# Kernel optimization log

Measured on AMD Instinct MI355X. Metric: run time of the kernel, lower is better.

## Reference

```python
import jax, jax.numpy as jnp
import numpy as np

NEG_INF = -1e30  # stand-in for float('-inf') masked_fill (safe for softmax)


def setup_inputs() -> dict:
    key = jax.random.key(0)
    ks = jax.random.split(key, 7)
    B, T, C, H, D = 4, 2048, 64, 6, 64
    s = 1.0 / np.sqrt(C)
    return {
        "x": jax.random.normal(ks[0], (B, T, C), dtype=jnp.float32),
        "y": jax.random.normal(ks[1], (B, T, C), dtype=jnp.float32),
        "Wq": jax.random.normal(ks[2], (H, C, D), dtype=jnp.float32) * s,
        "Wk": jax.random.normal(ks[3], (H, C, D), dtype=jnp.float32) * s,
        "Wv": jax.random.normal(ks[4], (H, C, D), dtype=jnp.float32) * s,
        "W_proj": jax.random.normal(ks[5], (H * D, C), dtype=jnp.float32) * (1.0 / np.sqrt(H * D)),
        "b_proj": jnp.zeros((C,), dtype=jnp.float32),
    }


def reference(x, y, Wq, Wk, Wv, W_proj, b_proj):
    # x, y: [B, T, C]; per-head projections stacked over H (heads vectorized).
    B, T, C = x.shape
    H, _, D = Wq.shape
    q = jnp.einsum("btc,hcd->bhtd", x, Wq)   # query from decoder input x
    k = jnp.einsum("btc,hcd->bhtd", y, Wk)   # key from encoder output y
    v = jnp.einsum("btc,hcd->bhtd", y, Wv)
    scale = D ** (-0.5)
    wei = jnp.einsum("bhtd,bhsd->bhts", q, k) * scale  # [B,H,T,T]
    # triu(ones(T,T), diagonal=1) future mask (causal)
    future = jnp.triu(jnp.ones((T, T), dtype=bool), k=1)
    wei = jnp.where(future, NEG_INF, wei)
    wei = jax.nn.softmax(wei, axis=-1)  # dropout = identity in eval
    out = jnp.einsum("bhts,bhsd->bhtd", wei, v)          # [B,H,T,D]
    out = out.transpose(0, 2, 1, 3).reshape(B, T, H * D)  # concat heads
    return out @ W_proj + b_proj                          # [B,T,C]
```

## Files before the change

kernel.cpp:

```cpp
#include <hip/hip_runtime.h>


typedef unsigned short u16t;
typedef __attribute__((ext_vector_type(8))) short short8;
typedef __attribute__((ext_vector_type(4))) float float4v;

#define MFMA16(a, b, c) __builtin_amdgcn_mfma_f32_16x16x32_bf16((a), (b), (c), 0, 0, 0)

union U8 { short8 s; unsigned u[4]; };

__device__ __forceinline__ float fexp2(float x) {
  return __builtin_amdgcn_exp2f(x);
}
__device__ __forceinline__ u16t f2bf(float f) {
  unsigned u = __float_as_uint(f);
  u += 0x7fffu + ((u >> 16) & 1u);
  return (u16t)(u >> 16);
}
__device__ __forceinline__ unsigned bftr(float f) {
  return __float_as_uint(f) >> 16;
}
__device__ __forceinline__ short8 load8_f32_bf16(const float* p) {
  float4 f0 = *(const float4*)p;
  float4 f1 = *(const float4*)(p + 4);
  short8 r;
  r[0] = (short)f2bf(f0.x); r[1] = (short)f2bf(f0.y);
  r[2] = (short)f2bf(f0.z); r[3] = (short)f2bf(f0.w);
  r[4] = (short)f2bf(f1.x); r[5] = (short)f2bf(f1.y);
  r[6] = (short)f2bf(f1.z); r[7] = (short)f2bf(f1.w);
  return r;
}

constexpr int Bb = 4, Tt = 2048, Cc = 64, Hh = 6, Dd = 64;
constexpr int BH = Bb * Hh;
constexpr int NQT = Tt / 64;
constexpr int LDT = 72;
constexpr int LDV = 136;
constexpr int OST = 65;
#define QSCALE (0.125f * 1.44269504088896f)

__global__ __launch_bounds__(256) void qkv_kernel(
    const float* __restrict__ x, const float* __restrict__ y,
    const float* __restrict__ Wq, const float* __restrict__ Wk,
    const float* __restrict__ Wv,
    u16t* __restrict__ Q, u16t* __restrict__ K, u16t* __restrict__ Vt) {
  __shared__ __align__(16) u16t wtq[64 * LDT];
  __shared__ __align__(16) u16t wtk[64 * LDT];
  __shared__ __align__(16) u16t wtv[64 * LDT];

  int bid = blockIdx.x;
  int bh = bid >> 5, tt = bid & 31;
  int b = bh / Hh, h = bh - b * Hh;
  int tid = threadIdx.x;
  int w = tid >> 6, lane = tid & 63;
  int l15 = lane & 15, q4 = lane >> 4;

  {
    const float* wq = Wq + h * 4096 + tid * 16;
    const float* wk = Wk + h * 4096 + tid * 16;
    const float* wv = Wv + h * 4096 + tid * 16;
    int c0 = tid >> 2, d0 = (tid & 3) * 16;
#pragma unroll
    for (int j = 0; j < 4; ++j) {
      float4 fq = *(const float4*)(wq + j * 4);
      float4 fk = *(const float4*)(wk + j * 4);
      float4 fv = *(const float4*)(wv + j * 4);
      int dr = (d0 + j * 4) * LDT + c0;
      wtq[dr          ] = f2bf(fq.x); wtq[dr + 1 * LDT] = f2bf(fq.y);
      wtq[dr + 2 * LDT] = f2bf(fq.z); wtq[dr + 3 * LDT] = f2bf(fq.w);
      wtk[dr          ] = f2bf(fk.x); wtk[dr + 1 * LDT] = f2bf(fk.y);
      wtk[dr + 2 * LDT] = f2bf(fk.z); wtk[dr + 3 * LDT] = f2bf(fk.w);
      wtv[dr          ] = f2bf(fv.x); wtv[dr + 1 * LDT] = f2bf(fv.y);
      wtv[dr + 2 * LDT] = f2bf(fv.z); wtv[dr + 3 * LDT] = f2bf(fv.w);
    }
  }

  int trow = tt * 64 + w * 16 + l15;
  const float* xrow = x + ((size_t)b * Tt + trow) * Cc;
  const float* yrow = y + ((size_t)b * Tt + trow) * Cc;
  short8 xa[2], ya[2];
#pragma unroll
  for (int kc = 0; kc < 2; ++kc) {
    xa[kc] = load8_f32_bf16(xrow + kc * 32 + q4 * 8);
    ya[kc] = load8_f32_bf16(yrow + kc * 32 + q4 * 8);
  }
  __syncthreads();

  float4v qa4[4], ka4[4], va4[4];
#pragma unroll
  for (int nc = 0; nc < 4; ++nc) {
    qa4[nc] = (float4v){0.f, 0.f, 0.f, 0.f};
    ka4[nc] = (float4v){0.f, 0.f, 0.f, 0.f};
    va4[nc] = (float4v){0.f, 0.f, 0.f, 0.f};
  }
#pragma unroll
  for (int nc = 0; nc < 4; ++nc) {
#pragma unroll
    for (int kc = 0; kc < 2; ++kc) {
      int off = (nc * 16 + l15) * LDT + kc * 32 + q4 * 8;
      short8 bq = *(const short8*)&wtq[off];
      short8 bk = *(const short8*)&wtk[off];
      short8 bv = *(const short8*)&wtv[off];
      qa4[nc] = MFMA16(xa[kc], bq, qa4[nc]);
      ka4[nc] = MFMA16(ya[kc], bk, ka4[nc]);
      va4[nc] = MFMA16(ya[kc], bv, va4[nc]);
    }
  }
  __syncthreads();

#pragma unroll
  for (int reg = 0; reg < 4; ++reg) {
    int rloc = w * 16 + q4 * 4 + reg;
#pragma unroll
    for (int nc = 0; nc < 4; ++nc) {
      wtq[rloc * LDT + nc * 16 + l15] = f2bf(qa4[nc][reg] * QSCALE);
      wtk[rloc * LDT + nc * 16 + l15] = f2bf(ka4[nc][reg]);
      wtv[(nc * 16 + l15) * LDT + rloc] = f2bf(va4[nc][reg]);
    }
  }
  __syncthreads();

  size_t tilebase = ((size_t)bh * Tt + tt * 64) * Dd;
#pragma unroll
  for (int i = 0; i < 2; ++i) {
    int id = tid * 2 + i;
    int row = id >> 3, c8 = id & 7;
    *(uint4*)&Q[tilebase + row * 64 + c8 * 8] = *(const uint4*)&wtq[row * LDT + c8 * 8];
    *(uint4*)&K[tilebase + row * 64 + c8 * 8] = *(const uint4*)&wtk[row * LDT + c8 * 8];
    *(uint4*)&Vt[((size_t)bh * 64 + row) * Tt + tt * 64 + c8 * 8] =
        *(const uint4*)&wtv[row * LDT + c8 * 8];
  }
}

__global__ __launch_bounds__(256) void attn_kernel(
    const u16t* __restrict__ Q, const u16t* __restrict__ K,
    const u16t* __restrict__ Vt, u16t* __restrict__ att) {
  __shared__ __align__(16) unsigned char smem[128 * LDT * 2 + 64 * LDV * 2];
  u16t* Kl = (u16t*)smem;
  u16t* Vl = (u16t*)(smem + 128 * LDT * 2);
  float* Ol = (float*)smem;
  float* Ll = (float*)(smem + 64 * OST * 4);

  int bid = blockIdx.x;
  int bh = bid % BH;
  int qt = (NQT - 1) - bid / BH;
  int b = bh / Hh, h = bh - (bh / Hh) * Hh;
  int tid = threadIdx.x;
  int w = tid >> 6;
  int lane = tid & 63;
  int l15 = lane & 15, q4 = lane >> 4;

  short8 qf[4][2];
#pragma unroll
  for (int it = 0; it < 4; ++it) {
    const u16t* qb = Q + ((size_t)bh * Tt + qt * 64 + it * 16 + l15) * Dd;
    qf[it][0] = *(const short8*)(qb + q4 * 8);
    qf[it][1] = *(const short8*)(qb + 32 + q4 * 8);
  }

  float4v O[4][4];
#pragma unroll
  for (int it = 0; it < 4; ++it)
#pragma unroll
    for (int nc = 0; nc < 4; ++nc) O[it][nc] = (float4v){0.f, 0.f, 0.f, 0.f};
  float l_[4] = {0.f, 0.f, 0.f, 0.f};

  const u16t* Kbh = K + (size_t)bh * Tt * Dd;
  const u16t* Vbh = Vt + (size_t)bh * Dd * Tt;
  const int bsmax = qt >> 1;

  for (int bs = 0; bs <= bsmax; ++bs) {
    __syncthreads();
    {
      const u16t* ks = Kbh + (size_t)bs * 128 * 64;
      const u16t* vs = Vbh + bs * 128;
#pragma unroll
      for (int i = 0; i < 4; ++i) {
        int id = tid + i * 256;
        *(uint4*)&Kl[(id >> 3) * LDT + (id & 7) * 8] =
            *(const uint4*)(ks + (size_t)(id >> 3) * 64 + (id & 7) * 8);
        *(uint4*)&Vl[(id >> 4) * LDV + (id & 15) * 8] =
            *(const uint4*)(vs + (size_t)(id >> 4) * Tt + (id & 15) * 8);
      }
    }
    __syncthreads();

    bool d0 = (2 * bs == qt);
    bool s1 = (2 * bs + 1 > qt);
    bool d1 = (2 * bs + 1 == qt);

    short8 kf00 = *(const short8*)&Kl[(w * 16 + l15) * LDT + q4 * 8];
    short8 kf01 = *(const short8*)&Kl[(w * 16 + l15) * LDT + 32 + q4 * 8];
    short8 kf10 = kf00, kf11 = kf01;
    if (!s1) {
      kf10 = *(const short8*)&Kl[(64 + w * 16 + l15) * LDT + q4 * 8];
      kf11 = *(const short8*)&Kl[(64 + w * 16 + l15) * LDT + 32 + q4 * 8];
    }
    short8 vf[4];
#pragma unroll
    for (int nc = 0; nc < 4; ++nc) {
      U8 t;
      *(uint2*)&t.u[0] = *(const uint2*)&Vl[(nc * 16 + l15) * LDV + w * 16 + q4 * 4];
      *(uint2*)&t.u[2] = *(const uint2*)&Vl[(nc * 16 + l15) * LDV + 64 + w * 16 + q4 * 4];
      vf[nc] = t.s;
    }

    __builtin_amdgcn_s_setprio(1);
#pragma unroll
    for (int it = 0; it < 4; ++it) {
      if (d0 && w > it) continue;
      float4v S0 = (float4v){0.f, 0.f, 0.f, 0.f};
      S0 = MFMA16(kf00, qf[it][0], S0);
      S0 = MFMA16(kf01, qf[it][1], S0);
      bool m0 = d0 && (w == it);
      float p0[4], p1[4];
#pragma unroll
      for (int reg = 0; reg < 4; ++reg) {
        p0[reg] = (m0 && (q4 * 4 + reg) > l15) ? 0.f : fexp2(S0[reg]);
        l_[it] += p0[reg];
      }
      if (s1 || (d1 && w > it)) {
#pragma unroll
        for (int reg = 0; reg < 4; ++reg) p1[reg] = 0.f;
      } else {
        float4v S1 = (float4v){0.f, 0.f, 0.f, 0.f};
        S1 = MFMA16(kf10, qf[it][0], S1);
        S1 = MFMA16(kf11, qf[it][1], S1);
        bool m1 = d1 && (w == it);
#pragma unroll
        for (int reg = 0; reg < 4; ++reg) {
          p1[reg] = (m1 && (q4 * 4 + reg) > l15) ? 0.f : fexp2(S1[reg]);
          l_[it] += p1[reg];
        }
      }
      U8 pa;
      pa.u[0] = bftr(p0[0]) | (bftr(p0[1]) << 16);
      pa.u[1] = bftr(p0[2]) | (bftr(p0[3]) << 16);
      pa.u[2] = bftr(p1[0]) | (bftr(p1[1]) << 16);
      pa.u[3] = bftr(p1[2]) | (bftr(p1[3]) << 16);
#pragma unroll
      for (int nc = 0; nc < 4; ++nc)
        O[it][nc] = MFMA16(pa.s, vf[nc], O[it][nc]);
    }
    __builtin_amdgcn_s_setprio(0);
  }

#pragma unroll
  for (int it = 0; it < 4; ++it) {
    l_[it] += __shfl_xor(l_[it], 16);
    l_[it] += __shfl_xor(l_[it], 32);
  }

  __syncthreads();
#pragma unroll
  for (int r = 0; r < 4; ++r) {
#pragma unroll
    for (int itc = 0; itc < 4; ++itc) {
      if (((itc - w) & 3) == r) {
#pragma unroll
        for (int nc = 0; nc < 4; ++nc)
#pragma unroll
          for (int reg = 0; reg < 4; ++reg) {
            int addr = (itc * 16 + q4 * 4 + reg) * OST + nc * 16 + l15;
            if (r == 0) Ol[addr] = O[itc][nc][reg];
            else        Ol[addr] += O[itc][nc][reg];
          }
        if (q4 == 0) {
          if (r == 0) Ll[itc * 16 + l15] = l_[itc];
          else        Ll[itc * 16 + l15] += l_[itc];
        }
      }
    }
    __syncthreads();
  }

#pragma unroll
  for (int i = 0; i < 2; ++i) {
    int id = tid * 2 + i;
    int row = id >> 3, c8 = id & 7;
    float inv = 1.0f / Ll[row];
    const float* orow = &Ol[row * OST + c8 * 8];
    U8 o;
#pragma unroll
    for (int k = 0; k < 4; ++k)
      o.u[k] = f2bf(orow[2 * k] * inv) | ((unsigned)f2bf(orow[2 * k + 1] * inv) << 16);
    int t = qt * 64 + row;
    *(uint4*)&att[((size_t)b * Tt + t) * (Hh * Dd) + h * Dd + c8 * 8] = *(const uint4*)&o;
  }
}

constexpr int LDP = 392;

__global__ __launch_bounds__(256) void proj_kernel(
    const u16t* __restrict__ att, const float* __restrict__ Wp,
    const float* __restrict__ bp, float* __restrict__ out) {
  __shared__ __align__(16) u16t wpt[64 * LDP];

  int bid = blockIdx.x;
  int tid = threadIdx.x;
  int w = tid >> 6, lane = tid & 63;
  int l15 = lane & 15, q4 = lane >> 4;
  int rt = w & 1, np = w >> 1;

#pragma unroll
  for (int i = 0; i < 24; ++i) {
    int idx = i * 1024 + tid * 4;
    float4 f = *(const float4*)(Wp + idx);
    int k = idx >> 6, n0 = idx & 63;
    int ad = n0 * LDP + k;
    wpt[ad          ] = f2bf(f.x); wpt[ad + 1 * LDP] = f2bf(f.y);
    wpt[ad + 2 * LDP] = f2bf(f.z); wpt[ad + 3 * LDP] = f2bf(f.w);
  }
  __syncthreads();

  int row0 = bid * 32 + rt * 16;
  const u16t* arow = att + (size_t)(row0 + l15) * 384;

  float4v acc[2];
#pragma unroll
  for (int j = 0; j < 2; ++j) acc[j] = (float4v){0.f, 0.f, 0.f, 0.f};

#pragma unroll
  for (int kc = 0; kc < 12; ++kc) {
    short8 a = *(const short8*)(arow + kc * 32 + q4 * 8);
#pragma unroll
    for (int j = 0; j < 2; ++j) {
      int nc = np * 2 + j;
      short8 bfr = *(const short8*)&wpt[(nc * 16 + l15) * LDP + kc * 32 + q4 * 8];
      acc[j] = MFMA16(a, bfr, acc[j]);
    }
  }

  float bv[2];
#pragma unroll
  for (int j = 0; j < 2; ++j) bv[j] = bp[(np * 2 + j) * 16 + l15];
#pragma unroll
  for (int reg = 0; reg < 4; ++reg) {
    int t = row0 + q4 * 4 + reg;
    size_t obase = (size_t)t * 64;
#pragma unroll
    for (int j = 0; j < 2; ++j)
      out[obase + (np * 2 + j) * 16 + l15] = acc[j][reg] + bv[j];
  }
}

extern "C" void kernel_launch(void* const* d_in, const int* in_sizes, int n_in,
                              void* d_out, int out_size, void* d_ws, size_t ws_size,
                              hipStream_t stream) {
  const float* x  = (const float*)d_in[0];
  const float* y  = (const float*)d_in[1];
  const float* Wq = (const float*)d_in[2];
  const float* Wk = (const float*)d_in[3];
  const float* Wv = (const float*)d_in[4];
  const float* Wp = (const float*)d_in[5];
  const float* bp = (const float*)d_in[6];
  float* out = (float*)d_out;

  const size_t NBH = (size_t)BH * Tt * Dd;
  u16t* Qs   = (u16t*)d_ws;
  u16t* Ks   = Qs + NBH;
  u16t* Vts  = Ks + NBH;
  u16t* attb = Vts + NBH;

  qkv_kernel<<<BH * NQT, 256, 0, stream>>>(x, y, Wq, Wk, Wv, Qs, Ks, Vts);
  attn_kernel<<<BH * NQT, 256, 0, stream>>>(Qs, Ks, Vts, attb);
  proj_kernel<<<(Bb * Tt) / 32, 256, 0, stream>>>(attb, Wp, bp, out);
}
```

Baseline: 121.7 us.

## Process two query tiles per attention block to share K/V tile loads

The attention kernel now assigns a pair of adjacent 64-row query tiles to one 512-thread block. Waves 0-3 handle the first tile and waves 4-7 the second, and both reuse the same 128-key K/V tile staged in shared memory. This halves global K/V traffic and the number of shared-memory fill passes per query row, and folds the causal diagonal handling into the pair structure. In exchange the grid halves, with larger blocks, which may reduce scheduling flexibility and occupancy. The output reduction now uses a 128-row shared-memory buffer.

```diff
diff --git a/kernel.cpp b/kernel.cpp
--- a/kernel.cpp
+++ b/kernel.cpp
@@ -34,6 +34,7 @@
 constexpr int Bb = 4, Tt = 2048, Cc = 64, Hh = 6, Dd = 64;
 constexpr int BH = Bb * Hh;
 constexpr int NQT = Tt / 64;
+constexpr int NPAIR = NQT / 2;
 constexpr int LDT = 72;
 constexpr int LDV = 136;
 constexpr int OST = 65;
@@ -132,28 +133,30 @@
   }
 }
 
-__global__ __launch_bounds__(256) void attn_kernel(
+__global__ __launch_bounds__(512) void attn_kernel(
     const u16t* __restrict__ Q, const u16t* __restrict__ K,
     const u16t* __restrict__ Vt, u16t* __restrict__ att) {
   __shared__ __align__(16) unsigned char smem[128 * LDT * 2 + 64 * LDV * 2];
   u16t* Kl = (u16t*)smem;
   u16t* Vl = (u16t*)(smem + 128 * LDT * 2);
   float* Ol = (float*)smem;
-  float* Ll = (float*)(smem + 64 * OST * 4);
+  float* Ll = (float*)(smem + 128 * OST * 4);
 
   int bid = blockIdx.x;
   int bh = bid % BH;
-  int qt = (NQT - 1) - bid / BH;
+  int p = (NPAIR - 1) - bid / BH;
   int b = bh / Hh, h = bh - (bh / Hh) * Hh;
   int tid = threadIdx.x;
   int w = tid >> 6;
   int lane = tid & 63;
+  int wj = w & 3, qh = w >> 2;
   int l15 = lane & 15, q4 = lane >> 4;
+  int qtq = 2 * p + qh;
 
   short8 qf[4][2];
 #pragma unroll
   for (int it = 0; it < 4; ++it) {
-    const u16t* qb = Q + ((size_t)bh * Tt + qt * 64 + it * 16 + l15) * Dd;
+    const u16t* qb = Q + ((size_t)bh * Tt + qtq * 64 + it * 16 + l15) * Dd;
     qf[it][0] = *(const short8*)(qb + q4 * 8);
     qf[it][1] = *(const short8*)(qb + 32 + q4 * 8);
   }
@@ -167,16 +170,15 @@
 
   const u16t* Kbh = K + (size_t)bh * Tt * Dd;
   const u16t* Vbh = Vt + (size_t)bh * Dd * Tt;
-  const int bsmax = qt >> 1;
-
-  for (int bs = 0; bs <= bsmax; ++bs) {
+
+  for (int bs = 0; bs <= p; ++bs) {
     __syncthreads();
     {
       const u16t* ks = Kbh + (size_t)bs * 128 * 64;
       const u16t* vs = Vbh + bs * 128;
 #pragma unroll
-      for (int i = 0; i < 4; ++i) {
-        int id = tid + i * 256;
+      for (int i = 0; i < 2; ++i) {
+        int id = tid + i * 512;
         *(uint4*)&Kl[(id >> 3) * LDT + (id & 7) * 8] =
             *(const uint4*)(ks + (size_t)(id >> 3) * 64 + (id & 7) * 8);
         *(uint4*)&Vl[(id >> 4) * LDV + (id & 15) * 8] =
@@ -185,48 +187,49 @@
     }
     __syncthreads();
 
-    bool d0 = (2 * bs == qt);
-    bool s1 = (2 * bs + 1 > qt);
-    bool d1 = (2 * bs + 1 == qt);
-
-    short8 kf00 = *(const short8*)&Kl[(w * 16 + l15) * LDT + q4 * 8];
-    short8 kf01 = *(const short8*)&Kl[(w * 16 + l15) * LDT + 32 + q4 * 8];
+    bool diag = (bs == p);
+    bool d0 = diag && (qh == 0);
+    bool s1 = d0;
+    bool d1 = diag && (qh == 1);
+
+    short8 kf00 = *(const short8*)&Kl[(wj * 16 + l15) * LDT + q4 * 8];
+    short8 kf01 = *(const short8*)&Kl[(wj * 16 + l15) * LDT + 32 + q4 * 8];
     short8 kf10 = kf00, kf11 = kf01;
     if (!s1) {
-      kf10 = *(const short8*)&Kl[(64 + w * 16 + l15) * LDT + q4 * 8];
-      kf11 = *(const short8*)&Kl[(64 + w * 16 + l15) * LDT + 32 + q4 * 8];
+      kf10 = *(const short8*)&Kl[(64 + wj * 16 + l15) * LDT + q4 * 8];
+      kf11 = *(const short8*)&Kl[(64 + wj * 16 + l15) * LDT + 32 + q4 * 8];
     }
     short8 vf[4];
 #pragma unroll
     for (int nc = 0; nc < 4; ++nc) {
       U8 t;
-      *(uint2*)&t.u[0] = *(const uint2*)&Vl[(nc * 16 + l15) * LDV + w * 16 + q4 * 4];
-      *(uint2*)&t.u[2] = *(const uint2*)&Vl[(nc * 16 + l15) * LDV + 64 + w * 16 + q4 * 4];
+      *(uint2*)&t.u[0] = *(const uint2*)&Vl[(nc * 16 + l15) * LDV + wj * 16 + q4 * 4];
+      *(uint2*)&t.u[2] = *(const uint2*)&Vl[(nc * 16 + l15) * LDV + 64 + wj * 16 + q4 * 4];
       vf[nc] = t.s;
     }
 
     __builtin_amdgcn_s_setprio(1);
 #pragma unroll
     for (int it = 0; it < 4; ++it) {
-      if (d0 && w > it) continue;
+      if (d0 && wj > it) continue;
       float4v S0 = (float4v){0.f, 0.f, 0.f, 0.f};
       S0 = MFMA16(kf00, qf[it][0], S0);
       S0 = MFMA16(kf01, qf[it][1], S0);
-      bool m0 = d0 && (w == it);
+      bool m0 = d0 && (wj == it);
       float p0[4], p1[4];
 #pragma unroll
       for (int reg = 0; reg < 4; ++reg) {
         p0[reg] = (m0 && (q4 * 4 + reg) > l15) ? 0.f : fexp2(S0[reg]);
         l_[it] += p0[reg];
       }
-      if (s1 || (d1 && w > it)) {
+      if (s1 || (d1 && wj > it)) {
 #pragma unroll
         for (int reg = 0; reg < 4; ++reg) p1[reg] = 0.f;
       } else {
         float4v S1 = (float4v){0.f, 0.f, 0.f, 0.f};
         S1 = MFMA16(kf10, qf[it][0], S1);
         S1 = MFMA16(kf11, qf[it][1], S1);
-        bool m1 = d1 && (w == it);
+        bool m1 = d1 && (wj == it);
 #pragma unroll
         for (int reg = 0; reg < 4; ++reg) {
           p1[reg] = (m1 && (q4 * 4 + reg) > l15) ? 0.f : fexp2(S1[reg]);
@@ -256,18 +259,18 @@
   for (int r = 0; r < 4; ++r) {
 #pragma unroll
     for (int itc = 0; itc < 4; ++itc) {
-      if (((itc - w) & 3) == r) {
+      if (((itc - wj) & 3) == r) {
 #pragma unroll
         for (int nc = 0; nc < 4; ++nc)
 #pragma unroll
           for (int reg = 0; reg < 4; ++reg) {
-            int addr = (itc * 16 + q4 * 4 + reg) * OST + nc * 16 + l15;
+            int addr = (qh * 64 + itc * 16 + q4 * 4 + reg) * OST + nc * 16 + l15;
             if (r == 0) Ol[addr] = O[itc][nc][reg];
             else        Ol[addr] += O[itc][nc][reg];
           }
         if (q4 == 0) {
-          if (r == 0) Ll[itc * 16 + l15] = l_[itc];
-          else        Ll[itc * 16 + l15] += l_[itc];
+          if (r == 0) Ll[qh * 64 + itc * 16 + l15] = l_[itc];
+          else        Ll[qh * 64 + itc * 16 + l15] += l_[itc];
         }
       }
     }
@@ -284,7 +287,7 @@
 #pragma unroll
     for (int k = 0; k < 4; ++k)
       o.u[k] = f2bf(orow[2 * k] * inv) | ((unsigned)f2bf(orow[2 * k + 1] * inv) << 16);
-    int t = qt * 64 + row;
+    int t = p * 128 + row;
     *(uint4*)&att[((size_t)b * Tt + t) * (Hh * Dd) + h * Dd + c8 * 8] = *(const uint4*)&o;
   }
 }
@@ -363,6 +366,6 @@
   u16t* attb = Vts + NBH;
 
   qkv_kernel<<<BH * NQT, 256, 0, stream>>>(x, y, Wq, Wk, Wv, Qs, Ks, Vts);
-  attn_kernel<<<BH * NQT, 256, 0, stream>>>(Qs, Ks, Vts, attb);
+  attn_kernel<<<BH * NPAIR, 512, 0, stream>>>(Qs, Ks, Vts, attb);
   proj_kernel<<<(Bb * Tt) / 32, 256, 0, stream>>>(attb, Wp, bp, out);
 }
```

Result: no change. 123.2 us (+1.3%).

## Split off unmasked attention blocks and pre-convert projection weights to bf16 once

Applied to the files above, without the earlier changes.

The attention inner loop now has a fast path for key blocks fully below the diagonal. That path drops the per-element causal mask checks and branches and does a tree reduction of the row sums. The bf16 packing uses a single v_perm instead of shifts and ORs. The qkv kernel also writes a transposed bf16 copy of W_proj once, so each proj block loads it with wide uint4 copies instead of converting fp32 with scattered 2-byte LDS stores. This adds code size and an extra workspace buffer.

```diff
diff --git a/kernel.cpp b/kernel.cpp
--- a/kernel.cpp
+++ b/kernel.cpp
@@ -17,8 +17,9 @@
   u += 0x7fffu + ((u >> 16) & 1u);
   return (u16t)(u >> 16);
 }
-__device__ __forceinline__ unsigned bftr(float f) {
-  return __float_as_uint(f) >> 16;
+__device__ __forceinline__ unsigned pk2(float hi, float lo) {
+  return __builtin_amdgcn_perm(__float_as_uint(hi), __float_as_uint(lo),
+                               0x07060302u);
 }
 __device__ __forceinline__ short8 load8_f32_bf16(const float* p) {
   float4 f0 = *(const float4*)p;
@@ -42,8 +43,9 @@
 __global__ __launch_bounds__(256) void qkv_kernel(
     const float* __restrict__ x, const float* __restrict__ y,
     const float* __restrict__ Wq, const float* __restrict__ Wk,
-    const float* __restrict__ Wv,
-    u16t* __restrict__ Q, u16t* __restrict__ K, u16t* __restrict__ Vt) {
+    const float* __restrict__ Wv, const float* __restrict__ Wp,
+    u16t* __restrict__ Q, u16t* __restrict__ K, u16t* __restrict__ Vt,
+    u16t* __restrict__ Wpt) {
   __shared__ __align__(16) u16t wtq[64 * LDT];
   __shared__ __align__(16) u16t wtk[64 * LDT];
   __shared__ __align__(16) u16t wtv[64 * LDT];
@@ -54,6 +56,12 @@
   int tid = threadIdx.x;
   int w = tid >> 6, lane = tid & 63;
   int l15 = lane & 15, q4 = lane >> 4;
+
+  if (bid < 96) {
+    int idx = bid * 256 + tid;
+    int c = idx / 384, r = idx - c * 384;
+    Wpt[idx] = f2bf(Wp[r * 64 + c]);
+  }
 
   {
     const float* wq = Wq + h * 4096 + tid * 16;
@@ -185,17 +193,6 @@
     }
     __syncthreads();
 
-    bool d0 = (2 * bs == qt);
-    bool s1 = (2 * bs + 1 > qt);
-    bool d1 = (2 * bs + 1 == qt);
-
-    short8 kf00 = *(const short8*)&Kl[(w * 16 + l15) * LDT + q4 * 8];
-    short8 kf01 = *(const short8*)&Kl[(w * 16 + l15) * LDT + 32 + q4 * 8];
-    short8 kf10 = kf00, kf11 = kf01;
-    if (!s1) {
-      kf10 = *(const short8*)&Kl[(64 + w * 16 + l15) * LDT + q4 * 8];
-      kf11 = *(const short8*)&Kl[(64 + w * 16 + l15) * LDT + 32 + q4 * 8];
-    }
     short8 vf[4];
 #pragma unroll
     for (int nc = 0; nc < 4; ++nc) {
@@ -205,44 +202,91 @@
       vf[nc] = t.s;
     }
 
-    __builtin_amdgcn_s_setprio(1);
-#pragma unroll
-    for (int it = 0; it < 4; ++it) {
-      if (d0 && w > it) continue;
-      float4v S0 = (float4v){0.f, 0.f, 0.f, 0.f};
-      S0 = MFMA16(kf00, qf[it][0], S0);
-      S0 = MFMA16(kf01, qf[it][1], S0);
-      bool m0 = d0 && (w == it);
-      float p0[4], p1[4];
-#pragma unroll
-      for (int reg = 0; reg < 4; ++reg) {
-        p0[reg] = (m0 && (q4 * 4 + reg) > l15) ? 0.f : fexp2(S0[reg]);
-        l_[it] += p0[reg];
-      }
-      if (s1 || (d1 && w > it)) {
-#pragma unroll
-        for (int reg = 0; reg < 4; ++reg) p1[reg] = 0.f;
-      } else {
+    if (bs < bsmax) {
+      short8 kf00 = *(const short8*)&Kl[(w * 16 + l15) * LDT + q4 * 8];
+      short8 kf01 = *(const short8*)&Kl[(w * 16 + l15) * LDT + 32 + q4 * 8];
+      short8 kf10 = *(const short8*)&Kl[(64 + w * 16 + l15) * LDT + q4 * 8];
+      short8 kf11 = *(const short8*)&Kl[(64 + w * 16 + l15) * LDT + 32 + q4 * 8];
+
+      __builtin_amdgcn_s_setprio(1);
+#pragma unroll
+      for (int it = 0; it < 4; ++it) {
+        float4v S0 = (float4v){0.f, 0.f, 0.f, 0.f};
         float4v S1 = (float4v){0.f, 0.f, 0.f, 0.f};
+        S0 = MFMA16(kf00, qf[it][0], S0);
+        S0 = MFMA16(kf01, qf[it][1], S0);
         S1 = MFMA16(kf10, qf[it][0], S1);
         S1 = MFMA16(kf11, qf[it][1], S1);
-        bool m1 = d1 && (w == it);
+        float p0[4], p1[4];
 #pragma unroll
         for (int reg = 0; reg < 4; ++reg) {
-          p1[reg] = (m1 && (q4 * 4 + reg) > l15) ? 0.f : fexp2(S1[reg]);
-          l_[it] += p1[reg];
+          p0[reg] = fexp2(S0[reg]);
+          p1[reg] = fexp2(S1[reg]);
         }
+        l_[it] += ((p0[0] + p0[1]) + (p0[2] + p0[3])) +
+                  ((p1[0] + p1[1]) + (p1[2] + p1[3]));
+        U8 pa;
+        pa.u[0] = pk2(p0[1], p0[0]);
+        pa.u[1] = pk2(p0[3], p0[2]);
+        pa.u[2] = pk2(p1[1], p1[0]);
+        pa.u[3] = pk2(p1[3], p1[2]);
+#pragma unroll
+        for (int nc = 0; nc < 4; ++nc)
+          O[it][nc] = MFMA16(pa.s, vf[nc], O[it][nc]);
       }
-      U8 pa;
-      pa.u[0] = bftr(p0[0]) | (bftr(p0[1]) << 16);
-      pa.u[1] = bftr(p0[2]) | (bftr(p0[3]) << 16);
-      pa.u[2] = bftr(p1[0]) | (bftr(p1[1]) << 16);
-      pa.u[3] = bftr(p1[2]) | (bftr(p1[3]) << 16);
-#pragma unroll
-      for (int nc = 0; nc < 4; ++nc)
-        O[it][nc] = MFMA16(pa.s, vf[nc], O[it][nc]);
-    }
-    __builtin_amdgcn_s_setprio(0);
+      __builtin_amdgcn_s_setprio(0);
+    } else {
+      bool d0 = (2 * bs == qt);
+      bool s1 = (2 * bs + 1 > qt);
+      bool d1 = (2 * bs + 1 == qt);
+
+      short8 kf00 = *(const short8*)&Kl[(w * 16 + l15) * LDT + q4 * 8];
+      short8 kf01 = *(const short8*)&Kl[(w * 16 + l15) * LDT + 32 + q4 * 8];
+      short8 kf10 = kf00, kf11 = kf01;
+      if (!s1) {
+        kf10 = *(const short8*)&Kl[(64 + w * 16 + l15) * LDT + q4 * 8];
+        kf11 = *(const short8*)&Kl[(64 + w * 16 + l15) * LDT + 32 + q4 * 8];
+      }
+
+      __builtin_amdgcn_s_setprio(1);
+#pragma unroll
+      for (int it = 0; it < 4; ++it) {
+        if (d0 && w > it) continue;
+        float4v S0 = (float4v){0.f, 0.f, 0.f, 0.f};
+        S0 = MFMA16(kf00, qf[it][0], S0);
+        S0 = MFMA16(kf01, qf[it][1], S0);
+        bool m0 = d0 && (w == it);
+        float p0[4], p1[4];
+#pragma unroll
+        for (int reg = 0; reg < 4; ++reg) {
+          p0[reg] = (m0 && (q4 * 4 + reg) > l15) ? 0.f : fexp2(S0[reg]);
+          l_[it] += p0[reg];
+        }
+        if (s1 || (d1 && w > it)) {
+#pragma unroll
+          for (int reg = 0; reg < 4; ++reg) p1[reg] = 0.f;
+        } else {
+          float4v S1 = (float4v){0.f, 0.f, 0.f, 0.f};
+          S1 = MFMA16(kf10, qf[it][0], S1);
+          S1 = MFMA16(kf11, qf[it][1], S1);
+          bool m1 = d1 && (w == it);
+#pragma unroll
+          for (int reg = 0; reg < 4; ++reg) {
+            p1[reg] = (m1 && (q4 * 4 + reg) > l15) ? 0.f : fexp2(S1[reg]);
+            l_[it] += p1[reg];
+          }
+        }
+        U8 pa;
+        pa.u[0] = pk2(p0[1], p0[0]);
+        pa.u[1] = pk2(p0[3], p0[2]);
+        pa.u[2] = pk2(p1[1], p1[0]);
+        pa.u[3] = pk2(p1[3], p1[2]);
+#pragma unroll
+        for (int nc = 0; nc < 4; ++nc)
+          O[it][nc] = MFMA16(pa.s, vf[nc], O[it][nc]);
+      }
+      __builtin_amdgcn_s_setprio(0);
+    }
   }
 
 #pragma unroll
@@ -283,7 +327,8 @@
     U8 o;
 #pragma unroll
     for (int k = 0; k < 4; ++k)
-      o.u[k] = f2bf(orow[2 * k] * inv) | ((unsigned)f2bf(orow[2 * k + 1] * inv) << 16);
+      o.u[k] = (unsigned)f2bf(orow[2 * k] * inv) |
+               ((unsigned)f2bf(orow[2 * k + 1] * inv) << 16);
     int t = qt * 64 + row;
     *(uint4*)&att[((size_t)b * Tt + t) * (Hh * Dd) + h * Dd + c8 * 8] = *(const uint4*)&o;
   }
@@ -292,7 +337,7 @@
 constexpr int LDP = 392;
 
 __global__ __launch_bounds__(256) void proj_kernel(
-    const u16t* __restrict__ att, const float* __restrict__ Wp,
+    const u16t* __restrict__ att, const u16t* __restrict__ Wpt,
     const float* __restrict__ bp, float* __restrict__ out) {
   __shared__ __align__(16) u16t wpt[64 * LDP];
 
@@ -303,13 +348,10 @@
   int rt = w & 1, np = w >> 1;
 
 #pragma unroll
-  for (int i = 0; i < 24; ++i) {
-    int idx = i * 1024 + tid * 4;
-    float4 f = *(const float4*)(Wp + idx);
-    int k = idx >> 6, n0 = idx & 63;
-    int ad = n0 * LDP + k;
-    wpt[ad          ] = f2bf(f.x); wpt[ad + 1 * LDP] = f2bf(f.y);
-    wpt[ad + 2 * LDP] = f2bf(f.z); wpt[ad + 3 * LDP] = f2bf(f.w);
+  for (int i = 0; i < 12; ++i) {
+    int id = tid + i * 256;
+    int r = id / 48, c8 = id - r * 48;
+    *(uint4*)&wpt[r * LDP + c8 * 8] = *(const uint4*)(Wpt + id * 8);
   }
   __syncthreads();
 
@@ -361,8 +403,9 @@
   u16t* Ks   = Qs + NBH;
   u16t* Vts  = Ks + NBH;
   u16t* attb = Vts + NBH;
-
-  qkv_kernel<<<BH * NQT, 256, 0, stream>>>(x, y, Wq, Wk, Wv, Qs, Ks, Vts);
+  u16t* Wpt  = attb + NBH;
+
+  qkv_kernel<<<BH * NQT, 256, 0, stream>>>(x, y, Wq, Wk, Wv, Wp, Qs, Ks, Vts, Wpt);
   attn_kernel<<<BH * NQT, 256, 0, stream>>>(Qs, Ks, Vts, attb);
-  proj_kernel<<<(Bb * Tt) / 32, 256, 0, stream>>>(attb, Wp, bp, out);
-}
+  proj_kernel<<<(Bb * Tt) / 32, 256, 0, stream>>>(attb, Wpt, bp, out);
+}
```

Measured after the change: 131.0 us. 7.6% more time.
